# Kernel optimization log

Hardware: AMD Instinct MI355X
Metric: run time of the kernel (lower is better)

Reference implementation:

```python
import jax, jax.numpy as jnp
import numpy as np

NEG_SLOPE = 0.2  # PyG GATv2Conv default

N_NODES = 10000
N_EDGES = 320000
DIM_IN = 128
DIM_H = 32
HEADS = 8
DIM_OUT = 32
HID = DIM_H * HEADS  # 256


def _gatv2(x, src, dst, Wl, Wr, att, bias, heads, ch, n):
    # x: [N, Fin]; src/dst: [E] (self-loops already included)
    xl = (x @ Wl).reshape(n, heads, ch)  # source-side transform
    xr = (x @ Wr).reshape(n, heads, ch)  # target-side transform
    e = jax.nn.leaky_relu(xl[src] + xr[dst], NEG_SLOPE)       # [E, H, C]
    score = jnp.einsum('ehc,hc->eh', e, att)                  # [E, H]
    m = jax.ops.segment_max(score, dst, num_segments=n)        # [N, H]
    ex = jnp.exp(score - m[dst])
    denom = jax.ops.segment_sum(ex, dst, num_segments=n)
    alpha = ex / (denom[dst] + 1e-16)                          # [E, H]
    out = jax.ops.segment_sum(alpha[:, :, None] * xl[src], dst, num_segments=n)
    return out.reshape(n, heads * ch) + bias


def setup_inputs() -> dict:
    key = jax.random.key(0)
    ks = jax.random.split(key, 16)
    x = jax.random.normal(ks[0], (N_NODES, DIM_IN), dtype=jnp.float32)
    edge_index = jax.random.randint(ks[1], (2, N_EDGES), 0, N_NODES, dtype=jnp.int64)

    def glorot(k, shape, fan_in):
        return jax.random.normal(k, shape, dtype=jnp.float32) * (1.0 / np.sqrt(fan_in))

    return {
        'x': x,
        'W1l': glorot(ks[2], (DIM_IN, HID), DIM_IN),
        'W1r': glorot(ks[3], (DIM_IN, HID), DIM_IN),
        'a1': glorot(ks[4], (HEADS, DIM_H), DIM_H),
        'b1': jnp.zeros((HID,), dtype=jnp.float32),
        'W2l': glorot(ks[5], (HID, HID), HID),
        'W2r': glorot(ks[6], (HID, HID), HID),
        'a2': glorot(ks[7], (HEADS, DIM_H), DIM_H),
        'b2': jnp.zeros((HID,), dtype=jnp.float32),
        'W3l': glorot(ks[8], (HID, DIM_OUT), HID),
        'W3r': glorot(ks[9], (HID, DIM_OUT), HID),
        'a3': glorot(ks[10], (1, DIM_OUT), DIM_OUT),
        'b3': jnp.zeros((DIM_OUT,), dtype=jnp.float32),
        'edge_index': edge_index,
    }


def reference(x, W1l, W1r, a1, b1, W2l, W2r, a2, b2, W3l, W3r, a3, b3, edge_index):
    n = x.shape[0]
    loops = jnp.arange(n, dtype=edge_index.dtype)
    src = jnp.concatenate([edge_index[0], loops])
    dst = jnp.concatenate([edge_index[1], loops])

    # eval mode: dropout(p=0.6) is identity
    h = _gatv2(x, src, dst, W1l, W1r, a1, b1, HEADS, DIM_H, n)
    h = jax.nn.relu(h)
    h_res = h
    h = _gatv2(h, src, dst, W2l, W2r, a2, b2, HEADS, DIM_H, n)
    h = h + h_res
    h = _gatv2(h, src, dst, W3l, W3r, a3, b3, 1, DIM_OUT, n)
    return h
```

## Files before the change

kernel.cpp:

```cpp
#include <hip/hip_runtime.h>

#define N_NODES 10000
#define N_EDGES 320000
#define E_TOT   (N_EDGES + N_NODES)
#define HID 256
#define NEG_SLOPE 0.2f
#define SLOTS 192

typedef __attribute__((ext_vector_type(8))) short short8;
typedef __attribute__((ext_vector_type(4))) float float4v;

__device__ int   g_cnt[N_NODES];
__device__ int   g_csr[(size_t)N_NODES * SLOTS];
__device__ __align__(16) float g_xl[(size_t)N_NODES * HID];
__device__ __align__(16) float g_xr[(size_t)N_NODES * HID];
__device__ __align__(16) float g_h1[(size_t)N_NODES * HID];
__device__ __align__(16) unsigned short g_xlb[(size_t)N_NODES * HID];
__device__ __align__(16) unsigned short g_abf[(size_t)N_NODES * 512];
__device__ __align__(16) unsigned short g_bp1a[16 * 8  * 64 * 8];
__device__ __align__(16) unsigned short g_bp2a[16 * 8  * 64 * 8];
__device__ __align__(16) unsigned short g_bp1b[16 * 16 * 64 * 8];
__device__ __align__(16) unsigned short g_bp2b[16 * 16 * 64 * 8];
__device__ __align__(16) unsigned short g_bp1c[2  * 16 * 64 * 8];
__device__ __align__(16) unsigned short g_bp2c[2  * 16 * 64 * 8];

#define LOG2E 1.44269504088896340736f

__device__ __forceinline__ unsigned short f2bf(float f) {
    unsigned int u = __float_as_uint(f);
    unsigned int r = (u + 0x7fffu + ((u >> 16) & 1u)) >> 16;
    return (unsigned short)r;
}
__device__ __forceinline__ float bf2f(unsigned short h) {
    return __uint_as_float(((unsigned int)h) << 16);
}
__device__ __forceinline__ unsigned int splitpack(float f) {
    unsigned short hi = f2bf(f);
    unsigned short lo = f2bf(f - bf2f(hi));
    return ((unsigned int)lo << 16) | hi;
}

__device__ __forceinline__ void packB(const float* __restrict__ B,
                                      unsigned short* __restrict__ Bp,
                                      int t, int nkc, int N) {
    int lane = t & 63;
    int kc   = (t >> 6) % nkc;
    int nt   = (t >> 6) / nkc;
    int n = nt * 16 + (lane & 15);
    int kbase = kc * 32 + (lane >> 4) * 8;
    #pragma unroll
    for (int j = 0; j < 8; ++j) {
        int kp = kbase + j;
        int k  = kp >> 1;
        float f = B[(size_t)k * N + n];
        unsigned short hi = f2bf(f);
        Bp[(size_t)t * 8 + j] = (kp & 1) ? f2bf(f - bf2f(hi)) : hi;
    }
}

__global__ __launch_bounds__(256) void k_prep(const float* __restrict__ W1l,
                                              const float* __restrict__ W1r,
                                              const float* __restrict__ W2l,
                                              const float* __restrict__ W2r,
                                              const float* __restrict__ W3l,
                                              const float* __restrict__ W3r,
                                              int* __restrict__ cnt) {
    const int S0 = 16 * 8 * 64;
    const int S1 = 16 * 16 * 64;
    const int S2 = 2 * 16 * 64;
    int t = blockIdx.x * blockDim.x + threadIdx.x;
    if (t < S0) {
        packB(W1l, g_bp1a, t, 8, 256);
        packB(W1r, g_bp2a, t, 8, 256);
    } else if (t < S0 + S1) {
        int u = t - S0;
        packB(W2l, g_bp1b, u, 16, 256);
        packB(W2r, g_bp2b, u, 16, 256);
    } else if (t < S0 + S1 + S2) {
        int u = t - S0 - S1;
        packB(W3l, g_bp1c, u, 16, 32);
        packB(W3r, g_bp2c, u, 16, 32);
    } else {
        int u = t - S0 - S1 - S2;
        if (u < N_NODES) cnt[u] = 0;
    }
}

#define FILL_BLOCKS ((E_TOT + 255) / 256)
__global__ __launch_bounds__(256) void k_fill_gemm1(
    const int* __restrict__ ei,
    int* __restrict__ cnt, int* __restrict__ csr,
    const float4* __restrict__ A4,
    const short8* __restrict__ Bp1, const short8* __restrict__ Bp2,
    unsigned short* __restrict__ C1b,
    float* __restrict__ C2)
{
    if (blockIdx.x < FILL_BLOCKS) {
        int e = blockIdx.x * 256 + threadIdx.x;
        if (e < E_TOT) {
            int src, dst;
            if (e < N_EDGES) { src = ei[e]; dst = ei[N_EDGES + e]; }
            else             { src = dst = e - N_EDGES; }
            int pos = atomicAdd(&cnt[dst], 1);
            if (pos < SLOTS) csr[dst * SLOTS + pos] = src;
        }
        return;
    }
    const int nkc = 8;
    int mt   = blockIdx.x - FILL_BLOCKS;
    int lane = threadIdx.x & 63;
    int wid  = threadIdx.x >> 6;
    int quad = lane >> 4;
    int col  = lane & 15;
    int r0 = mt * 32 + col;       if (r0 >= N_NODES) r0 = N_NODES - 1;
    int r1 = mt * 32 + 16 + col;  if (r1 >= N_NODES) r1 = N_NODES - 1;
    const float4* a0 = A4 + (size_t)r0 * 32 + quad;
    const float4* a1 = A4 + (size_t)r1 * 32 + quad;
    float4v acc[2][4][2];
    #pragma unroll
    for (int s = 0; s < 2; ++s)
        #pragma unroll
        for (int t = 0; t < 4; ++t) { acc[s][t][0] = (float4v)(0.f); acc[s][t][1] = (float4v)(0.f); }
    for (int kc = 0; kc < nkc; ++kc) {
        float4 v0 = a0[kc * 4];
        float4 v1 = a1[kc * 4];
        union { short8 s; unsigned int u[4]; } c0, c1;
        c0.u[0] = splitpack(v0.x); c0.u[1] = splitpack(v0.y);
        c0.u[2] = splitpack(v0.z); c0.u[3] = splitpack(v0.w);
        c1.u[0] = splitpack(v1.x); c1.u[1] = splitpack(v1.y);
        c1.u[2] = splitpack(v1.z); c1.u[3] = splitpack(v1.w);
        short8 A0 = c0.s, A1 = c1.s;
        #pragma unroll
        for (int t = 0; t < 4; ++t) {
            int nt = wid * 4 + t;
            size_t bi = ((size_t)(nt * nkc + kc)) * 64 + lane;
            short8 b1 = Bp1[bi];
            short8 b2 = Bp2[bi];
            acc[0][t][0] = __builtin_amdgcn_mfma_f32_16x16x32_bf16(A0, b1, acc[0][t][0], 0, 0, 0);
            acc[0][t][1] = __builtin_amdgcn_mfma_f32_16x16x32_bf16(A0, b2, acc[0][t][1], 0, 0, 0);
            acc[1][t][0] = __builtin_amdgcn_mfma_f32_16x16x32_bf16(A1, b1, acc[1][t][0], 0, 0, 0);
            acc[1][t][1] = __builtin_amdgcn_mfma_f32_16x16x32_bf16(A1, b2, acc[1][t][1], 0, 0, 0);
        }
    }
    #pragma unroll
    for (int s = 0; s < 2; ++s) {
        #pragma unroll
        for (int t = 0; t < 4; ++t) {
            int gc = (wid * 4 + t) * 16 + col;
            #pragma unroll
            for (int r = 0; r < 4; ++r) {
                int row = mt * 32 + s * 16 + quad * 4 + r;
                if (row < N_NODES) {
                    C1b[(size_t)row * 256 + gc] = f2bf(acc[s][t][0][r]);
                    C2[(size_t)row * 256 + gc]  = acc[s][t][1][r];
                }
            }
        }
    }
}

__global__ __launch_bounds__(256) void k_mgemm2(const short8* __restrict__ Af,
                                                const short8* __restrict__ Bp1,
                                                const short8* __restrict__ Bp2,
                                                unsigned short* __restrict__ C1b,
                                                float* __restrict__ C2,
                                                int Kp, int nkc) {
    int mt   = blockIdx.x;
    int lane = threadIdx.x & 63;
    int wid  = threadIdx.x >> 6;
    int quad = lane >> 4;
    int col  = lane & 15;
    int ks   = Kp >> 3;
    int r0 = mt * 32 + col;       if (r0 >= N_NODES) r0 = N_NODES - 1;
    int r1 = mt * 32 + 16 + col;  if (r1 >= N_NODES) r1 = N_NODES - 1;
    const short8* a0 = Af + (size_t)r0 * ks + quad;
    const short8* a1 = Af + (size_t)r1 * ks + quad;
    float4v acc[2][4][2];
    #pragma unroll
    for (int s = 0; s < 2; ++s)
        #pragma unroll
        for (int t = 0; t < 4; ++t) { acc[s][t][0] = (float4v)(0.f); acc[s][t][1] = (float4v)(0.f); }
    for (int kc = 0; kc < nkc; ++kc) {
        short8 A0 = a0[kc * 4];
        short8 A1 = a1[kc * 4];
        #pragma unroll
        for (int t = 0; t < 4; ++t) {
            int nt = wid * 4 + t;
            size_t bi = ((size_t)(nt * nkc + kc)) * 64 + lane;
            short8 b1 = Bp1[bi];
            short8 b2 = Bp2[bi];
            acc[0][t][0] = __builtin_amdgcn_mfma_f32_16x16x32_bf16(A0, b1, acc[0][t][0], 0, 0, 0);
            acc[0][t][1] = __builtin_amdgcn_mfma_f32_16x16x32_bf16(A0, b2, acc[0][t][1], 0, 0, 0);
            acc[1][t][0] = __builtin_amdgcn_mfma_f32_16x16x32_bf16(A1, b1, acc[1][t][0], 0, 0, 0);
            acc[1][t][1] = __builtin_amdgcn_mfma_f32_16x16x32_bf16(A1, b2, acc[1][t][1], 0, 0, 0);
        }
    }
    #pragma unroll
    for (int s = 0; s < 2; ++s) {
        #pragma unroll
        for (int t = 0; t < 4; ++t) {
            int gc = (wid * 4 + t) * 16 + col;
            #pragma unroll
            for (int r = 0; r < 4; ++r) {
                int row = mt * 32 + s * 16 + quad * 4 + r;
                if (row < N_NODES) {
                    C1b[(size_t)row * 256 + gc] = f2bf(acc[s][t][0][r]);
                    C2[(size_t)row * 256 + gc]  = acc[s][t][1][r];
                }
            }
        }
    }
}

__global__ __launch_bounds__(256) void k_mgemm32(const short8* __restrict__ Af,
                                                 const short8* __restrict__ Bp1,
                                                 const short8* __restrict__ Bp2,
                                                 float* __restrict__ C1,
                                                 float* __restrict__ C2) {
    int mt   = blockIdx.x;
    int lane = threadIdx.x & 63;
    int wid  = threadIdx.x >> 6;
    int quad = lane >> 4;
    int col  = lane & 15;
    int nt   = wid & 1;
    const short8* Bp = (wid < 2) ? Bp1 : Bp2;
    float* C = (wid < 2) ? C1 : C2;

    const short8* abase = Af + (size_t)(mt * 16 + col) * 64 + quad;
    float4v acc = (float4v)(0.f);
    #pragma unroll 4
    for (int kc = 0; kc < 16; ++kc) {
        short8 a = abase[kc * 4];
        short8 b = Bp[((size_t)(nt * 16 + kc)) * 64 + lane];
        acc = __builtin_amdgcn_mfma_f32_16x16x32_bf16(a, b, acc, 0, 0, 0);
    }
    #pragma unroll
    for (int r = 0; r < 4; ++r)
        C[(size_t)(mt * 16 + quad * 4 + r) * 32 + nt * 16 + col] = acc[r];
}

__global__ __launch_bounds__(256) void k_agg8(const unsigned short* __restrict__ xlb,
                                              const float4* __restrict__ xr4,
                                              const float4* __restrict__ att4,
                                              const float4* __restrict__ bias4,
                                              const int* __restrict__ cnt,
                                              const int* __restrict__ csr_src,
                                              const float4* __restrict__ res4,
                                              float4* __restrict__ out4,
                                              uint4* __restrict__ abf_out,
                                              int mode) {
    __shared__ float  ss[4][64];
    __shared__ float4 sacc[4][64];
    int node = blockIdx.x;
    int lane = threadIdx.x & 63;
    int wid  = threadIdx.x >> 6;
    float4 xrv = xr4[(size_t)node * 64 + lane];
    float4 av  = att4[lane];
    av.x *= LOG2E; av.y *= LOG2E; av.z *= LOG2E; av.w *= LOG2E;
    int c = cnt[node]; if (c > SLOTS) c = SLOTS;
    int start = node * SLOTS, end = start + c;
    int span = (c + 3) >> 2;
    int wbeg = start + wid * span;
    int wend = wbeg + span; if (wend > end) wend = end;
    int nloc = wend - wbeg;

    int ldi = wbeg + lane;
    int idxv = csr_src[ldi < end ? ldi : (end - 1)];

    float s = 0.f;
    float4 acc = make_float4(0.f, 0.f, 0.f, 0.f);

    for (int j0 = 0; j0 < nloc; j0 += 4) {
        int srcs[4];
        ushort4 uv[4];
        #pragma unroll
        for (int j = 0; j < 4; ++j)
            srcs[j] = __shfl(idxv, j0 + j);
        #pragma unroll
        for (int j = 0; j < 4; ++j)
            uv[j] = *(const ushort4*)(xlb + (size_t)srcs[j] * 256 + 4 * lane);
        #pragma unroll
        for (int j = 0; j < 4; ++j) {
            if (j0 + j < nloc) {
                float4 xv;
                xv.x = bf2f(uv[j].x); xv.y = bf2f(uv[j].y);
                xv.z = bf2f(uv[j].z); xv.w = bf2f(uv[j].w);
                float tx = xv.x + xrv.x, ty = xv.y + xrv.y;
                float tz = xv.z + xrv.z, tw = xv.w + xrv.w;
                float w = fmaxf(tx, NEG_SLOPE * tx) * av.x
                        + fmaxf(ty, NEG_SLOPE * ty) * av.y
                        + fmaxf(tz, NEG_SLOPE * tz) * av.z
                        + fmaxf(tw, NEG_SLOPE * tw) * av.w;
                w += __shfl_xor(w, 1);
                w += __shfl_xor(w, 2);
                w += __shfl_xor(w, 4);
                float p = exp2f(w);
                s += p;
                acc.x += p * xv.x;
                acc.y += p * xv.y;
                acc.z += p * xv.z;
                acc.w += p * xv.w;
            }
        }
    }
    ss[wid][lane] = s;
    sacc[wid][lane] = acc;
    __syncthreads();
    if (wid == 0) {
        float S = ss[0][lane] + ss[1][lane] + ss[2][lane] + ss[3][lane];
        float4 A = make_float4(0.f, 0.f, 0.f, 0.f);
        #pragma unroll
        for (int w = 0; w < 4; ++w) {
            float4 a = sacc[w][lane];
            A.x += a.x; A.y += a.y; A.z += a.z; A.w += a.w;
        }
        float inv = 1.f / (S + 1e-16f);
        float4 bv = bias4[lane];
        float4 o;
        o.x = A.x * inv + bv.x; o.y = A.y * inv + bv.y;
        o.z = A.z * inv + bv.z; o.w = A.w * inv + bv.w;
        if (mode == 0) {
            o.x = fmaxf(o.x, 0.f); o.y = fmaxf(o.y, 0.f);
            o.z = fmaxf(o.z, 0.f); o.w = fmaxf(o.w, 0.f);
        } else {
            float4 r = res4[(size_t)node * 64 + lane];
            o.x += r.x; o.y += r.y; o.z += r.z; o.w += r.w;
        }
        if (out4) out4[(size_t)node * 64 + lane] = o;
        if (abf_out) {
            uint4 u;
            u.x = splitpack(o.x); u.y = splitpack(o.y);
            u.z = splitpack(o.z); u.w = splitpack(o.w);
            abf_out[(size_t)node * 64 + lane] = u;
        }
    }
}

__global__ __launch_bounds__(256) void k_agg1(const float4* __restrict__ xl4,
                                              const float4* __restrict__ xr4,
                                              const float4* __restrict__ att4,
                                              const float4* __restrict__ bias4,
                                              const int* __restrict__ cnt,
                                              const int* __restrict__ csr_src,
                                              float4* __restrict__ out4) {
    int node = blockIdx.x * 4 + (threadIdx.x >> 6);
    if (node >= N_NODES) return;
    int lane = threadIdx.x & 63;
    int q = lane & 7;
    int grp = lane >> 3;
    float4 xrv = xr4[(size_t)node * 8 + q];
    float4 av  = att4[q];
    av.x *= LOG2E; av.y *= LOG2E; av.z *= LOG2E; av.w *= LOG2E;
    int c = cnt[node]; if (c > SLOTS) c = SLOTS;
    int start = node * SLOTS, end = start + c;
    float s = 0.f;
    float4 acc = make_float4(0.f, 0.f, 0.f, 0.f);
    for (int i = start + grp; i < end; i += 8) {
        int src = csr_src[i];
        float4 xv = xl4[(size_t)src * 8 + q];
        float tx = xv.x + xrv.x, ty = xv.y + xrv.y;
        float tz = xv.z + xrv.z, tw = xv.w + xrv.w;
        float w = fmaxf(tx, NEG_SLOPE * tx) * av.x
                + fmaxf(ty, NEG_SLOPE * ty) * av.y
                + fmaxf(tz, NEG_SLOPE * tz) * av.z
                + fmaxf(tw, NEG_SLOPE * tw) * av.w;
        w += __shfl_xor(w, 1);
        w += __shfl_xor(w, 2);
        w += __shfl_xor(w, 4);
        float p = exp2f(w);
        s += p;
        acc.x += p * xv.x;
        acc.y += p * xv.y;
        acc.z += p * xv.z;
        acc.w += p * xv.w;
    }
    #pragma unroll
    for (int off = 8; off < 64; off <<= 1) {
        s     += __shfl_xor(s, off);
        acc.x += __shfl_xor(acc.x, off);
        acc.y += __shfl_xor(acc.y, off);
        acc.z += __shfl_xor(acc.z, off);
        acc.w += __shfl_xor(acc.w, off);
    }
    if (grp == 0) {
        float inv = 1.f / (s + 1e-16f);
        float4 bv = bias4[q];
        float4 o;
        o.x = acc.x * inv + bv.x; o.y = acc.y * inv + bv.y;
        o.z = acc.z * inv + bv.z; o.w = acc.w * inv + bv.w;
        out4[(size_t)node * 8 + q] = o;
    }
}


extern "C" void kernel_launch(void* const* d_in, const int* in_sizes, int n_in,
                              void* d_out, int out_size, void* d_ws, size_t ws_size,
                              hipStream_t stream) {
    const float* x   = (const float*)d_in[0];
    const float* W1l = (const float*)d_in[1];
    const float* W1r = (const float*)d_in[2];
    const float* a1  = (const float*)d_in[3];
    const float* b1  = (const float*)d_in[4];
    const float* W2l = (const float*)d_in[5];
    const float* W2r = (const float*)d_in[6];
    const float* a2  = (const float*)d_in[7];
    const float* b2  = (const float*)d_in[8];
    const float* W3l = (const float*)d_in[9];
    const float* W3r = (const float*)d_in[10];
    const float* a3  = (const float*)d_in[11];
    const float* b3  = (const float*)d_in[12];
    const int*   ei  = (const int*)d_in[13];
    float* out = (float*)d_out;

    int *cnt, *csr;
    float *xl, *xr, *h1;
    unsigned short *xlb, *abf, *bp1a, *bp2a, *bp1b, *bp2b, *bp1c, *bp2c;
    hipGetSymbolAddress((void**)&cnt,    HIP_SYMBOL(g_cnt));
    hipGetSymbolAddress((void**)&csr,    HIP_SYMBOL(g_csr));
    hipGetSymbolAddress((void**)&xl,     HIP_SYMBOL(g_xl));
    hipGetSymbolAddress((void**)&xr,     HIP_SYMBOL(g_xr));
    hipGetSymbolAddress((void**)&h1,     HIP_SYMBOL(g_h1));
    hipGetSymbolAddress((void**)&xlb,    HIP_SYMBOL(g_xlb));
    hipGetSymbolAddress((void**)&abf,    HIP_SYMBOL(g_abf));
    hipGetSymbolAddress((void**)&bp1a,   HIP_SYMBOL(g_bp1a));
    hipGetSymbolAddress((void**)&bp2a,   HIP_SYMBOL(g_bp2a));
    hipGetSymbolAddress((void**)&bp1b,   HIP_SYMBOL(g_bp1b));
    hipGetSymbolAddress((void**)&bp2b,   HIP_SYMBOL(g_bp2b));
    hipGetSymbolAddress((void**)&bp1c,   HIP_SYMBOL(g_bp1c));
    hipGetSymbolAddress((void**)&bp2c,   HIP_SYMBOL(g_bp2c));

    k_prep<<<144, 256, 0, stream>>>(W1l, W1r, W2l, W2r, W3l, W3r, cnt);

    k_fill_gemm1<<<FILL_BLOCKS + (N_NODES + 31) / 32, 256, 0, stream>>>(
        ei, cnt, csr, (const float4*)x,
        (const short8*)bp1a, (const short8*)bp2a, xlb, xr);

    k_agg8<<<N_NODES, 256, 0, stream>>>(xlb, (const float4*)xr,
                                        (const float4*)a1, (const float4*)b1,
                                        cnt, csr, nullptr, (float4*)h1,
                                        (uint4*)abf, 0);

    k_mgemm2<<<(N_NODES + 31) / 32, 256, 0, stream>>>((const short8*)abf,
                                                      (const short8*)bp1b, (const short8*)bp2b,
                                                      xlb, xr, 512, 16);

    k_agg8<<<N_NODES, 256, 0, stream>>>(xlb, (const float4*)xr,
                                        (const float4*)a2, (const float4*)b2,
                                        cnt, csr, (const float4*)h1, nullptr,
                                        (uint4*)abf, 1);

    k_mgemm32<<<N_NODES / 16, 256, 0, stream>>>((const short8*)abf,
                                                (const short8*)bp1c, (const short8*)bp2c,
                                                xl, xr);

    k_agg1<<<(N_NODES + 3) / 4, 256, 0, stream>>>((const float4*)xl, (const float4*)xr,
                                                  (const float4*)a3, (const float4*)b3,
                                                  cnt, csr, (float4*)out);
}
```

Measured before the change: 224.3 us.

## Assign one node per wave in agg8 and move layer-2/3 weight packing into fill kernel

k_agg8 now processes one node per wavefront (four nodes per block) instead of splitting each node's edges across four waves. This removes the shared-memory cross-wave reduction and the __syncthreads. Separately, packing of the layer-2 and layer-3 weights moves out of k_prep into extra blocks of k_fill_gemm1, which shortens the serial prep kernel. The tradeoff is less memory-level parallelism per node, since each wave walks about 33 edges serially, and possible load imbalance across waves.

```diff
diff --git a/kernel.cpp b/kernel.cpp
--- a/kernel.cpp
+++ b/kernel.cpp
@@ -60,40 +60,30 @@
 
 __global__ __launch_bounds__(256) void k_prep(const float* __restrict__ W1l,
                                               const float* __restrict__ W1r,
-                                              const float* __restrict__ W2l,
-                                              const float* __restrict__ W2r,
-                                              const float* __restrict__ W3l,
-                                              const float* __restrict__ W3r,
                                               int* __restrict__ cnt) {
     const int S0 = 16 * 8 * 64;
-    const int S1 = 16 * 16 * 64;
-    const int S2 = 2 * 16 * 64;
     int t = blockIdx.x * blockDim.x + threadIdx.x;
     if (t < S0) {
         packB(W1l, g_bp1a, t, 8, 256);
         packB(W1r, g_bp2a, t, 8, 256);
-    } else if (t < S0 + S1) {
+    } else {
         int u = t - S0;
-        packB(W2l, g_bp1b, u, 16, 256);
-        packB(W2r, g_bp2b, u, 16, 256);
-    } else if (t < S0 + S1 + S2) {
-        int u = t - S0 - S1;
-        packB(W3l, g_bp1c, u, 16, 32);
-        packB(W3r, g_bp2c, u, 16, 32);
-    } else {
-        int u = t - S0 - S1 - S2;
         if (u < N_NODES) cnt[u] = 0;
     }
 }
 
-#define FILL_BLOCKS ((E_TOT + 255) / 256)
+#define FILL_BLOCKS  ((E_TOT + 255) / 256)
+#define GEMM1_BLOCKS ((N_NODES + 31) / 32)
+#define PACK2_BLOCKS ((16 * 16 * 64 + 2 * 16 * 64 + 255) / 256)
 __global__ __launch_bounds__(256) void k_fill_gemm1(
     const int* __restrict__ ei,
     int* __restrict__ cnt, int* __restrict__ csr,
     const float4* __restrict__ A4,
     const short8* __restrict__ Bp1, const short8* __restrict__ Bp2,
     unsigned short* __restrict__ C1b,
-    float* __restrict__ C2)
+    float* __restrict__ C2,
+    const float* __restrict__ W2l, const float* __restrict__ W2r,
+    const float* __restrict__ W3l, const float* __restrict__ W3r)
 {
     if (blockIdx.x < FILL_BLOCKS) {
         int e = blockIdx.x * 256 + threadIdx.x;
@@ -103,6 +93,22 @@
             else             { src = dst = e - N_EDGES; }
             int pos = atomicAdd(&cnt[dst], 1);
             if (pos < SLOTS) csr[dst * SLOTS + pos] = src;
+        }
+        return;
+    }
+    if (blockIdx.x >= FILL_BLOCKS + GEMM1_BLOCKS) {
+        const int S1 = 16 * 16 * 64;
+        const int S2 = 2 * 16 * 64;
+        int t = (blockIdx.x - FILL_BLOCKS - GEMM1_BLOCKS) * 256 + threadIdx.x;
+        if (t < S1) {
+            packB(W2l, g_bp1b, t, 16, 256);
+            packB(W2r, g_bp2b, t, 16, 256);
+        } else {
+            int u = t - S1;
+            if (u < S2) {
+                packB(W3l, g_bp1c, u, 16, 32);
+                packB(W3r, g_bp2c, u, 16, 32);
+            }
         }
         return;
     }
@@ -249,90 +255,75 @@
                                               float4* __restrict__ out4,
                                               uint4* __restrict__ abf_out,
                                               int mode) {
-    __shared__ float  ss[4][64];
-    __shared__ float4 sacc[4][64];
-    int node = blockIdx.x;
+    int node = blockIdx.x * 4 + (threadIdx.x >> 6);
+    if (node >= N_NODES) return;
     int lane = threadIdx.x & 63;
-    int wid  = threadIdx.x >> 6;
     float4 xrv = xr4[(size_t)node * 64 + lane];
     float4 av  = att4[lane];
     av.x *= LOG2E; av.y *= LOG2E; av.z *= LOG2E; av.w *= LOG2E;
     int c = cnt[node]; if (c > SLOTS) c = SLOTS;
-    int start = node * SLOTS, end = start + c;
-    int span = (c + 3) >> 2;
-    int wbeg = start + wid * span;
-    int wend = wbeg + span; if (wend > end) wend = end;
-    int nloc = wend - wbeg;
-
-    int ldi = wbeg + lane;
-    int idxv = csr_src[ldi < end ? ldi : (end - 1)];
+    int base0 = node * SLOTS;
 
     float s = 0.f;
     float4 acc = make_float4(0.f, 0.f, 0.f, 0.f);
 
-    for (int j0 = 0; j0 < nloc; j0 += 4) {
-        int srcs[4];
-        ushort4 uv[4];
-        #pragma unroll
-        for (int j = 0; j < 4; ++j)
-            srcs[j] = __shfl(idxv, j0 + j);
-        #pragma unroll
-        for (int j = 0; j < 4; ++j)
-            uv[j] = *(const ushort4*)(xlb + (size_t)srcs[j] * 256 + 4 * lane);
-        #pragma unroll
-        for (int j = 0; j < 4; ++j) {
-            if (j0 + j < nloc) {
-                float4 xv;
-                xv.x = bf2f(uv[j].x); xv.y = bf2f(uv[j].y);
-                xv.z = bf2f(uv[j].z); xv.w = bf2f(uv[j].w);
-                float tx = xv.x + xrv.x, ty = xv.y + xrv.y;
-                float tz = xv.z + xrv.z, tw = xv.w + xrv.w;
-                float w = fmaxf(tx, NEG_SLOPE * tx) * av.x
-                        + fmaxf(ty, NEG_SLOPE * ty) * av.y
-                        + fmaxf(tz, NEG_SLOPE * tz) * av.z
-                        + fmaxf(tw, NEG_SLOPE * tw) * av.w;
-                w += __shfl_xor(w, 1);
-                w += __shfl_xor(w, 2);
-                w += __shfl_xor(w, 4);
-                float p = exp2f(w);
-                s += p;
-                acc.x += p * xv.x;
-                acc.y += p * xv.y;
-                acc.z += p * xv.z;
-                acc.w += p * xv.w;
+    for (int base = 0; base < c; base += 64) {
+        int li = base + lane;
+        int idxv = csr_src[base0 + (li < c ? li : c - 1)];
+        int m = c - base; if (m > 64) m = 64;
+        for (int j0 = 0; j0 < m; j0 += 4) {
+            int srcs[4];
+            ushort4 uv[4];
+            #pragma unroll
+            for (int j = 0; j < 4; ++j)
+                srcs[j] = __shfl(idxv, j0 + j);
+            #pragma unroll
+            for (int j = 0; j < 4; ++j)
+                uv[j] = *(const ushort4*)(xlb + (size_t)srcs[j] * 256 + 4 * lane);
+            #pragma unroll
+            for (int j = 0; j < 4; ++j) {
+                if (j0 + j < m) {
+                    float4 xv;
+                    xv.x = bf2f(uv[j].x); xv.y = bf2f(uv[j].y);
+                    xv.z = bf2f(uv[j].z); xv.w = bf2f(uv[j].w);
+                    float tx = xv.x + xrv.x, ty = xv.y + xrv.y;
+                    float tz = xv.z + xrv.z, tw = xv.w + xrv.w;
+                    float w = fmaxf(tx, NEG_SLOPE * tx) * av.x
+                            + fmaxf(ty, NEG_SLOPE * ty) * av.y
+                            + fmaxf(tz, NEG_SLOPE * tz) * av.z
+                            + fmaxf(tw, NEG_SLOPE * tw) * av.w;
+                    w += __shfl_xor(w, 1);
+                    w += __shfl_xor(w, 2);
+                    w += __shfl_xor(w, 4);
+                    float p = exp2f(w);
+                    s += p;
+                    acc.x += p * xv.x;
+                    acc.y += p * xv.y;
+                    acc.z += p * xv.z;
+                    acc.w += p * xv.w;
+                }
             }
         }
     }
-    ss[wid][lane] = s;
-    sacc[wid][lane] = acc;
-    __syncthreads();
-    if (wid == 0) {
-        float S = ss[0][lane] + ss[1][lane] + ss[2][lane] + ss[3][lane];
-        float4 A = make_float4(0.f, 0.f, 0.f, 0.f);
-        #pragma unroll
-        for (int w = 0; w < 4; ++w) {
-            float4 a = sacc[w][lane];
-            A.x += a.x; A.y += a.y; A.z += a.z; A.w += a.w;
-        }
-        float inv = 1.f / (S + 1e-16f);
-        float4 bv = bias4[lane];
-        float4 o;
-        o.x = A.x * inv + bv.x; o.y = A.y * inv + bv.y;
-        o.z = A.z * inv + bv.z; o.w = A.w * inv + bv.w;
-        if (mode == 0) {
-            o.x = fmaxf(o.x, 0.f); o.y = fmaxf(o.y, 0.f);
-            o.z = fmaxf(o.z, 0.f); o.w = fmaxf(o.w, 0.f);
-        } else {
-            float4 r = res4[(size_t)node * 64 + lane];
-            o.x += r.x; o.y += r.y; o.z += r.z; o.w += r.w;
-        }
-        if (out4) out4[(size_t)node * 64 + lane] = o;
-        if (abf_out) {
-            uint4 u;
-            u.x = splitpack(o.x); u.y = splitpack(o.y);
-            u.z = splitpack(o.z); u.w = splitpack(o.w);
-            abf_out[(size_t)node * 64 + lane] = u;
-        }
+
+    float inv = 1.f / (s + 1e-16f);
+    float4 bv = bias4[lane];
+    float4 o;
+    o.x = acc.x * inv + bv.x; o.y = acc.y * inv + bv.y;
+    o.z = acc.z * inv + bv.z; o.w = acc.w * inv + bv.w;
+    if (mode == 0) {
+        o.x = fmaxf(o.x, 0.f); o.y = fmaxf(o.y, 0.f);
+        o.z = fmaxf(o.z, 0.f); o.w = fmaxf(o.w, 0.f);
+    } else {
+        float4 r = res4[(size_t)node * 64 + lane];
+        o.x += r.x; o.y += r.y; o.z += r.z; o.w += r.w;
+    }
+    if (out4) out4[(size_t)node * 64 + lane] = o;
+    if (abf_out) {
+        uint4 u;
+        u.x = splitpack(o.x); u.y = splitpack(o.y);
+        u.z = splitpack(o.z); u.w = splitpack(o.w);
+        abf_out[(size_t)node * 64 + lane] = u;
     }
 }
 
@@ -429,13 +420,14 @@
     hipGetSymbolAddress((void**)&bp1c,   HIP_SYMBOL(g_bp1c));
     hipGetSymbolAddress((void**)&bp2c,   HIP_SYMBOL(g_bp2c));
 
-    k_prep<<<144, 256, 0, stream>>>(W1l, W1r, W2l, W2r, W3l, W3r, cnt);
-
-    k_fill_gemm1<<<FILL_BLOCKS + (N_NODES + 31) / 32, 256, 0, stream>>>(
+    k_prep<<<(16 * 8 * 64 + N_NODES + 255) / 256, 256, 0, stream>>>(W1l, W1r, cnt);
+
+    k_fill_gemm1<<<FILL_BLOCKS + GEMM1_BLOCKS + PACK2_BLOCKS, 256, 0, stream>>>(
         ei, cnt, csr, (const float4*)x,
-        (const short8*)bp1a, (const short8*)bp2a, xlb, xr);
-
-    k_agg8<<<N_NODES, 256, 0, stream>>>(xlb, (const float4*)xr,
+        (const short8*)bp1a, (const short8*)bp2a, xlb, xr,
+        W2l, W2r, W3l, W3r);
+
+    k_agg8<<<(N_NODES + 3) / 4, 256, 0, stream>>>(xlb, (const float4*)xr,
                                         (const float4*)a1, (const float4*)b1,
                                         cnt, csr, nullptr, (float4*)h1,
                                         (uint4*)abf, 0);
@@ -444,7 +436,7 @@
                                                       (const short8*)bp1b, (const short8*)bp2b,
                                                       xlb, xr, 512, 16);
 
-    k_agg8<<<N_NODES, 256, 0, stream>>>(xlb, (const float4*)xr,
+    k_agg8<<<(N_NODES + 3) / 4, 256, 0, stream>>>(xlb, (const float4*)xr,
                                         (const float4*)a2, (const float4*)b2,
                                         cnt, csr, (const float4*)h1, nullptr,
                                         (uint4*)abf, 1);
```

Measured after the change: 227.1 us. No clear change (+1.2%).
